# Optimization experiments

Hardware: AMD Instinct MI355X
Metric: run time of the kernel (lower is better)

## Reference

```python
import jax, jax.numpy as jnp
import numpy as np

B, T, S, L_SRC, V, H, E, AV = 16, 128, 192, 192, 30522, 768, 768, 200
L_ORG = L_SRC - 1
KEEP, DEL, STOP, PAD = 3, 4, 2, 0  # SP_IDS = [KEEP, DEL, INSERT, STOP, PAD, LEFT, RIGHT, MARK]


def lstm(x, Wih, Whh, bih, bhh):
    # x: [B, T, E] -> outputs [B, T, H]; PyTorch gate order i, f, g, o
    Bx = x.shape[0]
    Hh = Whh.shape[1]
    def step(carry, xt):
        h, c = carry
        g = xt @ Wih.T + bih + h @ Whh.T + bhh
        i, f, gg, o = jnp.split(g, 4, axis=-1)
        c = jax.nn.sigmoid(f) * c + jax.nn.sigmoid(i) * jnp.tanh(gg)
        h = jax.nn.sigmoid(o) * jnp.tanh(c)
        return (h, c), h
    h0 = jnp.zeros((Bx, Hh), x.dtype)
    _, hs = jax.lax.scan(step, (h0, h0), jnp.swapaxes(x, 0, 1))
    return jnp.swapaxes(hs, 0, 1)


def compute_counters(input_edits, org_ids):
    # Vectorized replica of the host-side numpy counter bookkeeping.
    # Emits the PRE-update counters used at each timestep t (updated with gold = input_edits[:, t+1]).
    Bx = input_edits.shape[0]
    golds = jnp.swapaxes(input_edits[:, 1:], 0, 1)  # [T-1, B]
    barange = jnp.arange(Bx)
    Lorg = org_ids.shape[1]
    def step(carry, g):
        cd, ci, ca = carry
        pre = (cd, ci, ca)
        cd2 = cd + ((g == KEEP) | (g == DEL)).astype(jnp.int32)
        alive = (g != DEL) & (g != STOP) & (g != PAD)
        ci2 = ci + alive.astype(jnp.int32)
        nxt = jnp.clip(ca + 1, 0, Lorg - 1)
        tok = org_ids[barange, nxt]
        cond = alive & (g != KEEP) & (ca + 1 < Lorg) & ((tok == 103) | (tok == 3) | (tok == 4))
        ca2 = jnp.where(cond, ca + 1, jnp.maximum(cd2, ca))
        return (cd2, ci2, ca2), pre
    z = jnp.zeros((Bx,), jnp.int32)
    _, (cds, cis, cas) = jax.lax.scan(step, (z, z, z), golds)
    return jnp.swapaxes(cds, 0, 1), jnp.swapaxes(cis, 0, 1), jnp.swapaxes(cas, 0, 1)  # each [B, T-1]


def setup_inputs():
    key = jax.random.key(0)
    ks = jax.random.split(key, 40)
    s = 0.02
    rn = lambda k, sh: jax.random.normal(k, sh, jnp.float32) * s
    inp = {
        "input_edits": jax.random.randint(ks[0], (B, T), 0, 12),
        "input_actions": jax.random.randint(ks[1], (B, T), 0, AV),
        "simp_sent": jax.random.randint(ks[2], (B, S), 0, V),
        "org_ids": jax.random.randint(ks[3], (B, L_ORG), 0, V),
        "encoder_outputs_org": jax.random.normal(ks[4], (B, L_SRC, H), jnp.float32),
        "emb": rn(ks[5], (V, E)),
    }
    i = 6
    for nm in ("e", "a", "w"):
        inp["Wih_" + nm] = rn(ks[i], (4 * H, E)); i += 1
        inp["Whh_" + nm] = rn(ks[i], (4 * H, H)); i += 1
        inp["bih_" + nm] = jnp.zeros((4 * H,), jnp.float32)
        inp["bhh_" + nm] = jnp.zeros((4 * H,), jnp.float32)
    inp["W_align"] = rn(ks[i], (H, H)); i += 1
    inp["W_proj"] = rn(ks[i], (H, H)); i += 1
    inp["W_ref"] = rn(ks[i], (2, H)); i += 1
    inp["b_ref"] = jnp.zeros((2,), jnp.float32)
    inp["W_mlp"] = rn(ks[i], (E, 5 * H)); i += 1
    inp["b_mlp"] = jnp.zeros((E,), jnp.float32)
    inp["W_act"] = rn(ks[i], (E, 5 * H)); i += 1
    inp["b_act"] = jnp.zeros((E,), jnp.float32)
    inp["W_out"] = rn(ks[i], (V, E)); i += 1
    inp["b_out"] = jnp.zeros((V,), jnp.float32)
    inp["W_outact"] = rn(ks[i], (AV, E)); i += 1
    inp["b_outact"] = jnp.zeros((AV,), jnp.float32)
    m = np.full((1, AV), -100000.0, dtype=np.float32)
    m[0, [0, 1, 2, 5, 101, 102]] = 0.0
    inp["action_mask"] = jnp.asarray(m)
    return inp


def reference(input_edits, input_actions, simp_sent, org_ids, encoder_outputs_org, emb,
              Wih_e, Whh_e, bih_e, bhh_e, Wih_a, Whh_a, bih_a, bhh_a, Wih_w, Whh_w, bih_w, bhh_w,
              W_align, W_proj, W_ref, b_ref, W_mlp, b_mlp, W_act, b_act,
              W_out, b_out, W_outact, b_outact, action_mask):
    # tanh(output_hidden_alignment(enc)) then drop the first (CLS) position
    enc = jnp.tanh(encoder_outputs_org @ W_align.T)[:, 1:]  # [B, L_ORG, H]
    out_e = lstm(emb[input_edits], Wih_e, Whh_e, bih_e, bhh_e)
    out_a = lstm(emb[input_actions], Wih_a, Whh_a, bih_a, bhh_a)
    out_w = lstm(emb[simp_sent], Wih_w, Whh_w, bih_w, bhh_w)
    cd, ci, ca = compute_counters(input_edits, org_ids)  # [B, T-1] each
    Tm1 = input_edits.shape[1] - 1
    bidx = jnp.arange(enc.shape[0])[:, None]
    c_input = enc[bidx, cd]   # [B, T-1, H] data-dependent gather per timestep
    c_anno = enc[bidx, ca]
    c_word = out_w[bidx, ci]
    dec_e = out_e[:, :Tm1]
    dec_a = out_a[:, :Tm1]
    c_pair = jnp.stack([c_input, c_anno], axis=2)  # [B, T-1, 2, H]
    wref_e = jax.nn.softmax(dec_e @ W_ref.T + b_ref, axis=-1)
    wref_a = jax.nn.softmax(dec_a @ W_ref.T + b_ref, axis=-1)
    c_edit = jnp.einsum('btk,btkh->bth', wref_e, c_pair)
    c_action = jnp.einsum('btk,btkh->bth', wref_a, c_pair)
    attn = jax.nn.softmax(jnp.einsum('bth,blh->btl', c_word @ W_proj.T, enc), axis=-1)
    applied = jnp.einsum('btl,blh->bth', attn, enc)
    feat_a = jnp.concatenate([dec_a, dec_e, applied, c_action, c_word], axis=-1)
    act_log = jax.nn.log_softmax(jnp.tanh(feat_a @ W_act.T + b_act) @ W_outact.T + b_outact + action_mask[0], axis=-1)
    feat_e = jnp.concatenate([dec_e, dec_a, applied, c_edit, c_word], axis=-1)
    edit_log = jax.nn.log_softmax(jnp.tanh(feat_e @ W_mlp.T + b_mlp) @ W_out.T + b_out, axis=-1)
    return edit_log, act_log
```

## Files before the change

### kernel.cpp

```cpp
#include <hip/hip_runtime.h>
#include <hip/hip_bf16.h>

typedef __hip_bfloat16 bf16;

#define B_    16
#define T_    128
#define S_    192
#define H_    768
#define G4_   3072
#define V_    30522
#define AV_   200
#define L_    191
#define TM1_  127
#define R_    2032
#define K5_   3840
#define NB_   48
#define HSL_  16
#define NCV_  96

typedef short bf16x8_t __attribute__((ext_vector_type(8)));
typedef float f32x4_t  __attribute__((ext_vector_type(4)));

__device__ __forceinline__ float bf2f(bf16 v) { return __bfloat162float(v); }
__device__ __forceinline__ bf16  f2bf(float v) { return __float2bfloat16(v); }
__device__ __forceinline__ unsigned short f2us(float v) { bf16 h = f2bf(v); return *reinterpret_cast<unsigned short*>(&h); }
__device__ __forceinline__ float uslo(unsigned u) { union { unsigned i; float f; } x; x.i = u << 16; return x.f; }
__device__ __forceinline__ float ushi(unsigned u) { union { unsigned i; float f; } x; x.i = u & 0xffff0000u; return x.f; }
__device__ __forceinline__ float us2f(unsigned short u) { union { unsigned i; float f; } x; x.i = ((unsigned)u) << 16; return x.f; }
__device__ __forceinline__ float sigm(float x) { return 1.0f / (1.0f + expf(-x)); }

#define GLDS(gptr, lptr) \
    __builtin_amdgcn_global_load_lds((const __attribute__((address_space(1))) void*)(gptr), \
                                     (__attribute__((address_space(3))) void*)(lptr), 16, 0, 0)

__global__ __launch_bounds__(256) void gemm_mfma(
    const bf16* __restrict__ A, const bf16* __restrict__ W,
    const float* __restrict__ bias1, const float* __restrict__ bias2,
    bf16* __restrict__ Ch, float* __restrict__ Cf,
    int M, int N, int K, int act, int rowdiv, int lda)
{
    __shared__ short As[128 * 64];
    __shared__ short Ws[128 * 64];
    const int tid = threadIdx.x;
    const int wave = tid >> 6, lane = tid & 63;
    const int mw = (wave >> 1) * 64, nw = (wave & 1) * 64;
    const int bm = blockIdx.x * 128, bn = blockIdx.y * 128;

    const int schunk = (lane & 7) ^ (lane >> 3);

    const bf16* aSrc[4];
    const bf16* wSrc[4];
#pragma unroll
    for (int j = 0; j < 4; ++j) {
        const int idx = wave * 4 + j;
        const int srow = idx * 8 + (lane >> 3);
        int ga = bm + srow; if (ga > M - 1) ga = M - 1;
        const int ra = (rowdiv > 0) ? (ga + ga / rowdiv + 1) : ga;
        aSrc[j] = A + (size_t)ra * lda + schunk * 8;
        int gw = bn + srow; if (gw > N - 1) gw = N - 1;
        wSrc[j] = W + (size_t)gw * K + schunk * 8;
    }

    f32x4_t acc[4][4];
#pragma unroll
    for (int mi = 0; mi < 4; ++mi)
#pragma unroll
        for (int ni = 0; ni < 4; ++ni) acc[mi][ni] = (f32x4_t){0.f, 0.f, 0.f, 0.f};

    const int fr = lane & 15;
    const int fr7 = fr & 7;
    const int cq = lane >> 4;

    for (int k0 = 0; k0 < K; k0 += 64) {
#pragma unroll
        for (int j = 0; j < 4; ++j) {
            const int idx = wave * 4 + j;
            GLDS(aSrc[j] + k0, &As[idx * 512]);
            GLDS(wSrc[j] + k0, &Ws[idx * 512]);
        }
        __syncthreads();
#pragma unroll
        for (int half = 0; half < 2; ++half) {
            const int gc = half * 4 + cq;
            const int lc = (gc ^ fr7) * 8;
            bf16x8_t af[4], wf[4];
#pragma unroll
            for (int i = 0; i < 4; ++i)
                af[i] = *(const bf16x8_t*)&As[(mw + i * 16 + fr) * 64 + lc];
#pragma unroll
            for (int i = 0; i < 4; ++i)
                wf[i] = *(const bf16x8_t*)&Ws[(nw + i * 16 + fr) * 64 + lc];
#pragma unroll
            for (int mi = 0; mi < 4; ++mi)
#pragma unroll
                for (int ni = 0; ni < 4; ++ni)
                    acc[mi][ni] = __builtin_amdgcn_mfma_f32_16x16x32_bf16(af[mi], wf[ni], acc[mi][ni], 0, 0, 0);
        }
        __syncthreads();
    }

    const int cl = lane & 15;
    const int rg = (lane >> 4) * 4;
#pragma unroll
    for (int mi = 0; mi < 4; ++mi) {
#pragma unroll
        for (int ni = 0; ni < 4; ++ni) {
            const int col = bn + nw + ni * 16 + cl;
            if (col >= N) continue;
#pragma unroll
            for (int j = 0; j < 4; ++j) {
                const int row = bm + mw + mi * 16 + rg + j;
                if (row >= M) continue;
                float v = acc[mi][ni][j];
                if (bias1) v += bias1[col];
                if (bias2) v += bias2[col];
                if (act == 1) v = tanhf(v);
                if (Ch) Ch[(size_t)row * N + col] = f2bf(v);
                else    Cf[(size_t)row * N + col] = v;
            }
        }
    }
}

struct ConvJobs {
    const float* src[9];
    bf16* dst[9];
    int n4[9];
};
__global__ void conv_many_kernel(ConvJobs jobs)
{
    const int w = blockIdx.y;
    const int i = blockIdx.x * 256 + threadIdx.x;
    if (i >= jobs.n4[w]) return;
    const float* s = jobs.src[w];
    bf16* d = jobs.dst[w];
    float4 v = *(const float4*)(s + (size_t)i * 4);
    ushort4 o;
    o.x = f2us(v.x); o.y = f2us(v.y); o.z = f2us(v.z); o.w = f2us(v.w);
    *(ushort4*)(d + (size_t)i * 4) = o;
}

__global__ __launch_bounds__(256) void lstm_mfma_kernel(
    const bf16* __restrict__ pxe, const bf16* __restrict__ pxa, const bf16* __restrict__ pxw,
    const float* __restrict__ We, const float* __restrict__ Wa, const float* __restrict__ Ww,
    bf16* __restrict__ oute, bf16* __restrict__ outa, bf16* __restrict__ outw,
    unsigned short* __restrict__ hbuf, int* __restrict__ flags,
    const float* __restrict__ Wout, bf16* __restrict__ Wob)
{
    const int tid = threadIdx.x;

    if (blockIdx.x >= 3 * NB_) {
        const int wid = blockIdx.x - 3 * NB_;
        const int n4 = V_ * H_ / 4;
        for (int i = wid * 256 + tid; i < n4; i += NCV_ * 256) {
            float4 v = *(const float4*)(Wout + (size_t)i * 4);
            ushort4 o;
            o.x = f2us(v.x); o.y = f2us(v.y); o.z = f2us(v.z); o.w = f2us(v.w);
            *(ushort4*)(Wob + (size_t)i * 4) = o;
        }
        return;
    }

    const int which = blockIdx.x / NB_;
    const int nb = blockIdx.x % NB_;
    const bf16* px; const float* W; bf16* out; int Tn;
    if (which == 0)      { px = pxe; W = We; out = oute; Tn = T_; }
    else if (which == 1) { px = pxa; W = Wa; out = outa; Tn = T_; }
    else                 { px = pxw; W = Ww; out = outw; Tn = S_; }
    unsigned short* hG = hbuf + (size_t)which * (2 * B_ * H_);
    int* flg = flags + which * 64;

    const int wv = tid >> 6;
    const int lane = tid & 63;
    const int so = nb * HSL_;

    __shared__ unsigned short hL[16][776];
    __shared__ float gS[4][16][17];
    __shared__ unsigned short oring[8][16][16];

    bf16x8_t Afrag[24];
    {
        const int m = lane & 15;
        const int kb8 = (lane >> 4) * 8;
        const float* wrow = W + (size_t)(wv * H_ + so + m) * H_ + kb8;
#pragma unroll
        for (int kb = 0; kb < 24; ++kb) {
            float4 f0 = *(const float4*)(wrow + kb * 32);
            float4 f1 = *(const float4*)(wrow + kb * 32 + 4);
            bf16x8_t a;
            a[0] = (short)f2us(f0.x); a[1] = (short)f2us(f0.y);
            a[2] = (short)f2us(f0.z); a[3] = (short)f2us(f0.w);
            a[4] = (short)f2us(f1.x); a[5] = (short)f2us(f1.y);
            a[6] = (short)f2us(f1.z); a[7] = (short)f2us(f1.w);
            Afrag[kb] = a;
        }
    }

    for (int i = tid; i < 16 * 776; i += 256) ((unsigned short*)hL)[i] = 0;

    const int cb = tid >> 4;
    const int chl = tid & 15;
    float c = 0.f;

    const int bn = lane & 15;
    const int bk = (lane >> 4) * 8;

    unsigned short pxr0, pxr1, pxr2, pxr3;
    {
        const bf16* q = px + ((size_t)cb * Tn + 0) * G4_ + so + chl;
        pxr0 = *(const unsigned short*)(q);
        pxr1 = *(const unsigned short*)(q + H_);
        pxr2 = *(const unsigned short*)(q + 2 * H_);
        pxr3 = *(const unsigned short*)(q + 3 * H_);
    }

    int cur = 0;
    for (int step = 0; step < Tn; ++step) {
        if (step > 0) {
            const unsigned long long* hsrc =
                (const unsigned long long*)(hG + (size_t)cur * (B_ * H_));
            for (int i = tid; i < B_ * H_ / 4; i += 256) {
                const unsigned long long v =
                    __hip_atomic_load(hsrc + i, __ATOMIC_RELAXED, __HIP_MEMORY_SCOPE_AGENT);
                const int bb = i / (H_ / 4);
                const int cc = i - bb * (H_ / 4);
                ((unsigned long long*)&hL[bb][0])[cc] = v;
            }
        }
        __syncthreads();

        f32x4_t acc = {0.f, 0.f, 0.f, 0.f};
#pragma unroll
        for (int kb = 0; kb < 24; ++kb) {
            bf16x8_t bfr = *(const bf16x8_t*)&hL[bn][kb * 32 + bk];
            acc = __builtin_amdgcn_mfma_f32_16x16x32_bf16(Afrag[kb], bfr, acc, 0, 0, 0);
        }
        {
            const int m0 = (lane >> 4) * 4;
#pragma unroll
            for (int j = 0; j < 4; ++j) gS[wv][m0 + j][bn] = acc[j];
        }
        __syncthreads();

        {
            const float gi = gS[0][chl][cb] + us2f(pxr0);
            const float gf = gS[1][chl][cb] + us2f(pxr1);
            const float gg = gS[2][chl][cb] + us2f(pxr2);
            const float go = gS[3][chl][cb] + us2f(pxr3);
            const float cn = sigm(gf) * c + sigm(gi) * tanhf(gg);
            const float hn = sigm(go) * tanhf(cn);
            c = cn;
            oring[step & 7][cb][chl] = f2us(hn);
            __hip_atomic_store(&hG[(size_t)(cur ^ 1) * (B_ * H_) + cb * H_ + so + chl],
                               f2us(hn), __ATOMIC_RELAXED, __HIP_MEMORY_SCOPE_AGENT);
        }

        if (step + 1 < Tn) {
            __syncthreads();
            const int target = step + 1;
            if (tid == 0)
                __hip_atomic_store(&flg[nb], target, __ATOMIC_RELAXED, __HIP_MEMORY_SCOPE_AGENT);
            {
                const bf16* q = px + ((size_t)cb * Tn + target) * G4_ + so + chl;
                pxr0 = *(const unsigned short*)(q);
                pxr1 = *(const unsigned short*)(q + H_);
                pxr2 = *(const unsigned short*)(q + 2 * H_);
                pxr3 = *(const unsigned short*)(q + 3 * H_);
            }
            if ((step & 7) == 7) {
                const int base = step & ~7;
                for (int s2 = 0; s2 < 8; ++s2)
                    out[((size_t)cb * Tn + base + s2) * H_ + so + chl] =
                        *reinterpret_cast<const bf16*>(&oring[s2][cb][chl]);
            }
            if (lane < NB_) {
                long guard = 0;
                while (__hip_atomic_load(&flg[lane], __ATOMIC_RELAXED, __HIP_MEMORY_SCOPE_AGENT) < target) {
                    __builtin_amdgcn_s_sleep(1);
                    if (++guard > 50000000L) break;
                }
            }
        } else {
            const int base = step & ~7;
            const int cnt8 = (step & 7) + 1;
            for (int s2 = 0; s2 < cnt8; ++s2)
                out[((size_t)cb * Tn + base + s2) * H_ + so + chl] =
                    *reinterpret_cast<const bf16*>(&oring[s2][cb][chl]);
        }
        cur ^= 1;
    }
}

__global__ void gather3_kernel(const int* __restrict__ ids_e, const int* __restrict__ ids_a,
                               const int* __restrict__ ids_w, const float* __restrict__ emb,
                               bf16* __restrict__ oe, bf16* __restrict__ oa,
                               bf16* __restrict__ ow)
{
    const int which = blockIdx.y;
    const int r = blockIdx.x;
    const int* ids; bf16* out; int nr;
    if (which == 0)      { ids = ids_e; out = oe; nr = B_ * T_; }
    else if (which == 1) { ids = ids_a; out = oa; nr = B_ * T_; }
    else                 { ids = ids_w; out = ow; nr = B_ * S_; }
    if (r >= nr) return;
    const float4* src = (const float4*)(emb + (size_t)ids[r] * H_);
    ushort4* dst = (ushort4*)(out + (size_t)r * H_);
    for (int h = threadIdx.x; h < H_ / 4; h += 256) {
        float4 v = src[h];
        ushort4 o;
        o.x = f2us(v.x); o.y = f2us(v.y); o.z = f2us(v.z); o.w = f2us(v.w);
        dst[h] = o;
    }
}

__global__ void counters_kernel(const int* __restrict__ edits, const int* __restrict__ org,
                                int* __restrict__ cd, int* __restrict__ ci, int* __restrict__ ca)
{
    const int b = threadIdx.x;
    if (b >= B_) return;
    int vd = 0, vi = 0, va = 0;
    for (int t = 0; t < TM1_; ++t) {
        cd[b * TM1_ + t] = vd; ci[b * TM1_ + t] = vi; ca[b * TM1_ + t] = va;
        const int g = edits[b * T_ + t + 1];
        const int vd2 = vd + ((g == 3 || g == 4) ? 1 : 0);
        const int alive = (g != 4 && g != 2 && g != 0) ? 1 : 0;
        const int vi2 = vi + alive;
        int nxt = va + 1; if (nxt > L_ - 1) nxt = L_ - 1;
        const int tok = org[b * L_ + nxt];
        const bool cond = alive && (g != 3) && (va + 1 < L_) && (tok == 103 || tok == 3 || tok == 4);
        const int va2 = cond ? (va + 1) : max(vd2, va);
        vd = vd2; vi = vi2; va = va2;
    }
}

__global__ void gather_cword_kernel(const bf16* __restrict__ outw, const int* __restrict__ ci,
                                    bf16* __restrict__ cw)
{
    const int r = blockIdx.x;
    const int b = r / TM1_;
    const unsigned* src = (const unsigned*)(outw + ((size_t)b * S_ + ci[r]) * H_);
    unsigned* dst = (unsigned*)(cw + (size_t)r * H_);
    for (int h = threadIdx.x; h < H_ / 2; h += 256) dst[h] = src[h];
}

__global__ __launch_bounds__(256) void ref_combine_kernel(
    const bf16* __restrict__ oute, const bf16* __restrict__ outa, const bf16* __restrict__ enc,
    const float* __restrict__ Wref, const float* __restrict__ bref,
    const int* __restrict__ cd, const int* __restrict__ ca,
    bf16* __restrict__ ced, bf16* __restrict__ cac)
{
    const int r = blockIdx.x;
    const int b = r / TM1_;
    const int t = r % TM1_;
    const bf16* de = oute + ((size_t)b * T_ + t) * H_;
    const bf16* da = outa + ((size_t)b * T_ + t) * H_;
    const int tid = threadIdx.x;
    __shared__ float red[256][4];
    float s0 = 0.f, s1 = 0.f, s2 = 0.f, s3 = 0.f;
    for (int k = tid; k < H_; k += 256) {
        const float w0 = Wref[k];
        const float w1 = Wref[H_ + k];
        const float e = bf2f(de[k]);
        const float a = bf2f(da[k]);
        s0 += e * w0; s1 += e * w1; s2 += a * w0; s3 += a * w1;
    }
    red[tid][0] = s0; red[tid][1] = s1; red[tid][2] = s2; red[tid][3] = s3;
    __syncthreads();
    for (int off = 128; off > 0; off >>= 1) {
        if (tid < off) {
            red[tid][0] += red[tid + off][0];
            red[tid][1] += red[tid + off][1];
            red[tid][2] += red[tid + off][2];
            red[tid][3] += red[tid + off][3];
        }
        __syncthreads();
    }
    const float br0 = bref[0], br1 = bref[1];
    const float xe0 = red[0][0] + br0, xe1 = red[0][1] + br1;
    const float xa0 = red[0][2] + br0, xa1 = red[0][3] + br1;
    const float me = fmaxf(xe0, xe1);
    const float ee0 = expf(xe0 - me), ee1 = expf(xe1 - me);
    const float pe0 = ee0 / (ee0 + ee1), pe1 = ee1 / (ee0 + ee1);
    const float ma = fmaxf(xa0, xa1);
    const float ea0 = expf(xa0 - ma), ea1 = expf(xa1 - ma);
    const float pa0 = ea0 / (ea0 + ea1), pa1 = ea1 / (ea0 + ea1);

    const bf16* ei = enc + ((size_t)b * L_ + cd[r]) * H_;
    const bf16* ea = enc + ((size_t)b * L_ + ca[r]) * H_;
    for (int h = tid; h < H_; h += 256) {
        const float vi = bf2f(ei[h]);
        const float va = bf2f(ea[h]);
        ced[(size_t)r * H_ + h] = f2bf(pe0 * vi + pe1 * va);
        cac[(size_t)r * H_ + h] = f2bf(pa0 * vi + pa1 * va);
    }
}

__global__ __launch_bounds__(256) void attn_kernel(const bf16* __restrict__ q,
                                                   const bf16* __restrict__ enc,
                                                   bf16* __restrict__ app)
{
    const int r = blockIdx.x;
    const int b = r / TM1_;
    const int tid = threadIdx.x;
    __shared__ float qs[H_];
    __shared__ float p[L_ + 1];
    __shared__ float red[256];
    const bf16* qrow = q + (size_t)r * H_;
    for (int h = tid; h < H_; h += 256) qs[h] = bf2f(qrow[h]);
    __syncthreads();
    const bf16* eb = enc + (size_t)b * L_ * H_;
    float myv = -1e30f;
    if (tid < L_) {
        const unsigned* er = (const unsigned*)(eb + (size_t)tid * H_);
        float s = 0.f;
        for (int k2 = 0; k2 < H_ / 2; ++k2) {
            const unsigned u = er[k2];
            s += qs[2 * k2] * uslo(u) + qs[2 * k2 + 1] * ushi(u);
        }
        p[tid] = s;
        myv = s;
    }
    red[tid] = myv;
    __syncthreads();
    for (int off = 128; off > 0; off >>= 1) {
        if (tid < off) red[tid] = fmaxf(red[tid], red[tid + off]);
        __syncthreads();
    }
    const float m = red[0];
    __syncthreads();
    float e = 0.f;
    if (tid < L_) e = expf(p[tid] - m);
    red[tid] = e;
    __syncthreads();
    for (int off = 128; off > 0; off >>= 1) {
        if (tid < off) red[tid] += red[tid + off];
        __syncthreads();
    }
    const float invZ = 1.f / red[0];
    __syncthreads();
    if (tid < L_) p[tid] = e * invZ;
    __syncthreads();
    for (int h = tid; h < H_; h += 256) {
        float s = 0.f;
        for (int l = 0; l < L_; ++l) s += p[l] * bf2f(eb[(size_t)l * H_ + h]);
        app[(size_t)r * H_ + h] = f2bf(s);
    }
}

__global__ void feat_kernel(const bf16* __restrict__ oute, const bf16* __restrict__ outa,
                            const bf16* __restrict__ app, const bf16* __restrict__ ced,
                            const bf16* __restrict__ cac, const bf16* __restrict__ cw,
                            bf16* __restrict__ fe, bf16* __restrict__ fa)
{
    const int r = blockIdx.x;
    const int b = r / TM1_;
    const int t = r % TM1_;
    const unsigned* de  = (const unsigned*)(oute + ((size_t)b * T_ + t) * H_);
    const unsigned* da  = (const unsigned*)(outa + ((size_t)b * T_ + t) * H_);
    const unsigned* ap  = (const unsigned*)(app + (size_t)r * H_);
    const unsigned* ce  = (const unsigned*)(ced + (size_t)r * H_);
    const unsigned* cA  = (const unsigned*)(cac + (size_t)r * H_);
    const unsigned* cwp = (const unsigned*)(cw + (size_t)r * H_);
    unsigned* pfe = (unsigned*)(fe + (size_t)r * K5_);
    unsigned* pfa = (unsigned*)(fa + (size_t)r * K5_);
    const int HW = H_ / 2;
    for (int h = threadIdx.x; h < HW; h += 256) {
        const unsigned ve = de[h], va = da[h], vap = ap[h], vce = ce[h], vca = cA[h], vcw = cwp[h];
        pfe[h] = ve;  pfe[HW + h] = va;  pfe[2 * HW + h] = vap; pfe[3 * HW + h] = vce; pfe[4 * HW + h] = vcw;
        pfa[h] = va;  pfa[HW + h] = ve;  pfa[2 * HW + h] = vap; pfa[3 * HW + h] = vca; pfa[4 * HW + h] = vcw;
    }
}

__global__ __launch_bounds__(1024) void logsoftmax_edit_kernel(float* __restrict__ out)
{
    float* row = out + (size_t)blockIdx.x * V_;
    const int tid = threadIdx.x;
    const int lane = tid & 63;
    const int wid = tid >> 6;
    __shared__ unsigned short rowb[V_];
    __shared__ float wredm[16], wreds[16];
    __shared__ float fin;

    float m = -1e30f, s = 0.f;
    for (int i = tid; i < V_; i += 1024) {
        const float x = row[i];
        rowb[i] = f2us(x);
        if (x > m) { s = s * expf(m - x) + 1.f; m = x; }
        else s += expf(x - m);
    }
#pragma unroll
    for (int off = 32; off > 0; off >>= 1) {
        const float m2 = __shfl_down(m, off);
        const float s2 = __shfl_down(s, off);
        const float mn = fmaxf(m, m2);
        s = s * expf(m - mn) + s2 * expf(m2 - mn);
        m = mn;
    }
    if (lane == 0) { wredm[wid] = m; wreds[wid] = s; }
    __syncthreads();
    if (wid == 0) {
        m = (lane < 16) ? wredm[lane] : -1e30f;
        s = (lane < 16) ? wreds[lane] : 0.f;
#pragma unroll
        for (int off = 8; off > 0; off >>= 1) {
            const float m2 = __shfl_down(m, off);
            const float s2 = __shfl_down(s, off);
            const float mn = fmaxf(m, m2);
            s = s * expf(m - mn) + s2 * expf(m2 - mn);
            m = mn;
        }
        if (lane == 0) fin = m + logf(s);
    }
    __syncthreads();
    const float lz = fin;
    for (int i = tid; i < V_; i += 1024) row[i] = us2f(rowb[i]) - lz;
}

__global__ __launch_bounds__(256) void logsoftmax_act_kernel(const float* __restrict__ in,
                                                             float* __restrict__ out)
{
    const float* row = in + (size_t)blockIdx.x * AV_;
    float* orow = out + (size_t)blockIdx.x * AV_;
    const int tid = threadIdx.x;
    __shared__ float red[256];
    float m = -1e30f;
    if (tid < AV_) m = row[tid];
    red[tid] = m;
    __syncthreads();
    for (int off = 128; off > 0; off >>= 1) {
        if (tid < off) red[tid] = fmaxf(red[tid], red[tid + off]);
        __syncthreads();
    }
    m = red[0];
    __syncthreads();
    float s = 0.f;
    if (tid < AV_) s = expf(row[tid] - m);
    red[tid] = s;
    __syncthreads();
    for (int off = 128; off > 0; off >>= 1) {
        if (tid < off) red[tid] += red[tid + off];
        __syncthreads();
    }
    const float lz = m + logf(red[0]);
    if (tid < AV_) orow[tid] = row[tid] - lz;
}

extern "C" void kernel_launch(void* const* d_in, const int* in_sizes, int n_in,
                              void* d_out, int out_size, void* d_ws, size_t ws_size,
                              hipStream_t stream)
{
    const int* input_edits   = (const int*)d_in[0];
    const int* input_actions = (const int*)d_in[1];
    const int* simp_sent     = (const int*)d_in[2];
    const int* org_ids       = (const int*)d_in[3];
    const float* enc_org     = (const float*)d_in[4];
    const float* emb         = (const float*)d_in[5];
    const float* Wih_e = (const float*)d_in[6];
    const float* Whh_e = (const float*)d_in[7];
    const float* bih_e = (const float*)d_in[8];
    const float* bhh_e = (const float*)d_in[9];
    const float* Wih_a = (const float*)d_in[10];
    const float* Whh_a = (const float*)d_in[11];
    const float* bih_a = (const float*)d_in[12];
    const float* bhh_a = (const float*)d_in[13];
    const float* Wih_w = (const float*)d_in[14];
    const float* Whh_w = (const float*)d_in[15];
    const float* bih_w = (const float*)d_in[16];
    const float* bhh_w = (const float*)d_in[17];
    const float* W_align = (const float*)d_in[18];
    const float* W_proj  = (const float*)d_in[19];
    const float* W_ref   = (const float*)d_in[20];
    const float* b_ref   = (const float*)d_in[21];
    const float* W_mlp   = (const float*)d_in[22];
    const float* b_mlp   = (const float*)d_in[23];
    const float* W_act   = (const float*)d_in[24];
    const float* b_act   = (const float*)d_in[25];
    const float* W_out   = (const float*)d_in[26];
    const float* b_out   = (const float*)d_in[27];
    const float* W_outact = (const float*)d_in[28];
    const float* b_outact = (const float*)d_in[29];
    const float* action_mask = (const float*)d_in[30];

    float* out = (float*)d_out;
    float* edit_out = out;
    float* act_out  = out + (size_t)R_ * V_;

    char* p = (char*)d_ws;
    auto take = [&](size_t bytes) { void* q = (void*)p; p += ((bytes + 255) / 256) * 256; return q; };
    int* flags = (int*)take(3 * 256);
    unsigned short* hbuf = (unsigned short*)take((size_t)3 * 2 * B_ * H_ * 2);
    char* alias_base = p;
    bf16* xe   = (bf16*)take((size_t)B_ * T_ * H_ * 2);
    bf16* xa   = (bf16*)take((size_t)B_ * T_ * H_ * 2);
    bf16* xw   = (bf16*)take((size_t)B_ * S_ * H_ * 2);
    bf16* pxe  = (bf16*)take((size_t)B_ * T_ * G4_ * 2);
    bf16* pxa  = (bf16*)take((size_t)B_ * T_ * G4_ * 2);
    bf16* pxw  = (bf16*)take((size_t)B_ * S_ * G4_ * 2);
    bf16* oute = (bf16*)take((size_t)B_ * T_ * H_ * 2);
    bf16* outa = (bf16*)take((size_t)B_ * T_ * H_ * 2);
    bf16* outw = (bf16*)take((size_t)B_ * S_ * H_ * 2);
    bf16* enc  = (bf16*)take((size_t)B_ * L_ * H_ * 2);
    bf16* cw   = (bf16*)take((size_t)R_ * H_ * 2);
    bf16* ced  = (bf16*)take((size_t)R_ * H_ * 2);
    bf16* cac  = (bf16*)take((size_t)R_ * H_ * 2);
    bf16* qb   = (bf16*)take((size_t)R_ * H_ * 2);
    bf16* app  = (bf16*)take((size_t)R_ * H_ * 2);
    bf16* fe   = (bf16*)take((size_t)R_ * K5_ * 2);
    bf16* fa   = (bf16*)take((size_t)R_ * K5_ * 2);
    bf16* he   = (bf16*)take((size_t)R_ * H_ * 2);
    bf16* ha   = (bf16*)take((size_t)R_ * H_ * 2);
    int*  cd   = (int*)take((size_t)R_ * 4);
    int*  ci   = (int*)take((size_t)R_ * 4);
    int*  ca   = (int*)take((size_t)R_ * 4);
    float* actbuf = (float*)take((size_t)R_ * AV_ * 4);
    bf16* Wmlpb = (bf16*)take((size_t)H_ * K5_ * 2);
    bf16* Wactb = (bf16*)take((size_t)H_ * K5_ * 2);
    bf16* Woab  = (bf16*)take((size_t)AV_ * H_ * 2);
    bf16* Wob = (bf16*)alias_base;
    bf16* WihEb = fe;
    bf16* WihAb = fe + (size_t)G4_ * H_;
    bf16* WihWb = fe + (size_t)2 * G4_ * H_;
    bf16* encb   = fa;
    bf16* Walb   = fa + (size_t)B_ * S_ * H_;
    bf16* Wprojb = fa + (size_t)B_ * S_ * H_ + (size_t)H_ * H_;

    hipMemsetAsync(flags, 0, 3 * 256, stream);

    ConvJobs jobs;
    jobs.src[0] = Wih_e;   jobs.dst[0] = WihEb;  jobs.n4[0] = G4_ * H_ / 4;
    jobs.src[1] = Wih_a;   jobs.dst[1] = WihAb;  jobs.n4[1] = G4_ * H_ / 4;
    jobs.src[2] = Wih_w;   jobs.dst[2] = WihWb;  jobs.n4[2] = G4_ * H_ / 4;
    jobs.src[3] = W_mlp;   jobs.dst[3] = Wmlpb;  jobs.n4[3] = H_ * K5_ / 4;
    jobs.src[4] = W_act;   jobs.dst[4] = Wactb;  jobs.n4[4] = H_ * K5_ / 4;
    jobs.src[5] = enc_org; jobs.dst[5] = encb;   jobs.n4[5] = B_ * S_ * H_ / 4;
    jobs.src[6] = W_align; jobs.dst[6] = Walb;   jobs.n4[6] = H_ * H_ / 4;
    jobs.src[7] = W_proj;  jobs.dst[7] = Wprojb; jobs.n4[7] = H_ * H_ / 4;
    jobs.src[8] = W_outact;jobs.dst[8] = Woab;   jobs.n4[8] = AV_ * H_ / 4;
    conv_many_kernel<<<dim3((H_ * K5_ / 4 + 255) / 256, 9), 256, 0, stream>>>(jobs);

    gather3_kernel<<<dim3(B_ * S_, 3), 256, 0, stream>>>(
        input_edits, input_actions, simp_sent, emb, xe, xa, xw);

    dim3 gpx((B_ * T_ + 127) / 128, (G4_ + 127) / 128);
    gemm_mfma<<<gpx, 256, 0, stream>>>(xe, WihEb, bih_e, bhh_e, pxe, nullptr, B_ * T_, G4_, H_, 0, 0, H_);
    gemm_mfma<<<gpx, 256, 0, stream>>>(xa, WihAb, bih_a, bhh_a, pxa, nullptr, B_ * T_, G4_, H_, 0, 0, H_);
    dim3 gpxw((B_ * S_ + 127) / 128, (G4_ + 127) / 128);
    gemm_mfma<<<gpxw, 256, 0, stream>>>(xw, WihWb, bih_w, bhh_w, pxw, nullptr, B_ * S_, G4_, H_, 0, 0, H_);

    dim3 genc((B_ * L_ + 127) / 128, (H_ + 127) / 128);
    gemm_mfma<<<genc, 256, 0, stream>>>(encb, Walb, nullptr, nullptr, enc, nullptr, B_ * L_, H_, H_, 1, L_, H_);

    counters_kernel<<<1, 64, 0, stream>>>(input_edits, org_ids, cd, ci, ca);

    lstm_mfma_kernel<<<3 * NB_ + NCV_, 256, 0, stream>>>(pxe, pxa, pxw, Whh_e, Whh_a, Whh_w,
                                                         oute, outa, outw, hbuf, flags,
                                                         W_out, Wob);

    gather_cword_kernel<<<R_, 256, 0, stream>>>(outw, ci, cw);

    ref_combine_kernel<<<R_, 256, 0, stream>>>(oute, outa, enc, W_ref, b_ref, cd, ca, ced, cac);

    dim3 gproj((R_ + 127) / 128, (H_ + 127) / 128);
    gemm_mfma<<<gproj, 256, 0, stream>>>(cw, Wprojb, nullptr, nullptr, qb, nullptr, R_, H_, H_, 0, 0, H_);

    attn_kernel<<<R_, 256, 0, stream>>>(qb, enc, app);

    feat_kernel<<<R_, 256, 0, stream>>>(oute, outa, app, ced, cac, cw, fe, fa);

    gemm_mfma<<<gproj, 256, 0, stream>>>(fe, Wmlpb, b_mlp, nullptr, he, nullptr, R_, H_, K5_, 1, 0, K5_);
    gemm_mfma<<<gproj, 256, 0, stream>>>(fa, Wactb, b_act, nullptr, ha, nullptr, R_, H_, K5_, 1, 0, K5_);

    dim3 gact((R_ + 127) / 128, (AV_ + 127) / 128);
    gemm_mfma<<<gact, 256, 0, stream>>>(ha, Woab, b_outact, action_mask, nullptr, actbuf, R_, AV_, H_, 0, 0, H_);
    logsoftmax_act_kernel<<<R_, 256, 0, stream>>>(actbuf, act_out);

    dim3 gedit((R_ + 127) / 128, (V_ + 127) / 128);
    gemm_mfma<<<gedit, 256, 0, stream>>>(he, Wob, b_out, nullptr, nullptr, edit_out, R_, V_, H_, 0, 0, H_);
    logsoftmax_edit_kernel<<<R_, 1024, 0, stream>>>(edit_out);
}
```

Before: 2.138 ms.

## Fuse reference-combine, attention and feature assembly; gather c_word rows inside GEMM

Three per-row kernels (ref_combine, attention, feature concat) become one, which writes the concatenated feature rows directly. The c_word gather kernel is removed: the projection GEMM reads outw rows through a per-row index array that the counters kernel now also emits. This drops several launches and the global round-trips through the cw, ced, cac and app intermediate buffers. The GEMM gains an extra pointer check and an indirect row load.

```diff
diff --git a/kernel.cpp b/kernel.cpp
--- a/kernel.cpp
+++ b/kernel.cpp
@@ -37,7 +37,8 @@
     const bf16* __restrict__ A, const bf16* __restrict__ W,
     const float* __restrict__ bias1, const float* __restrict__ bias2,
     bf16* __restrict__ Ch, float* __restrict__ Cf,
-    int M, int N, int K, int act, int rowdiv, int lda)
+    int M, int N, int K, int act, int rowdiv, int lda,
+    const int* __restrict__ gidx)
 {
     __shared__ short As[128 * 64];
     __shared__ short Ws[128 * 64];
@@ -55,7 +56,9 @@
         const int idx = wave * 4 + j;
         const int srow = idx * 8 + (lane >> 3);
         int ga = bm + srow; if (ga > M - 1) ga = M - 1;
-        const int ra = (rowdiv > 0) ? (ga + ga / rowdiv + 1) : ga;
+        int ra;
+        if (gidx) ra = gidx[ga];
+        else ra = (rowdiv > 0) ? (ga + ga / rowdiv + 1) : ga;
         aSrc[j] = A + (size_t)ra * lda + schunk * 8;
         int gw = bn + srow; if (gw > N - 1) gw = N - 1;
         wSrc[j] = W + (size_t)gw * K + schunk * 8;
@@ -314,13 +317,15 @@
 }
 
 __global__ void counters_kernel(const int* __restrict__ edits, const int* __restrict__ org,
-                                int* __restrict__ cd, int* __restrict__ ci, int* __restrict__ ca)
+                                int* __restrict__ cd, int* __restrict__ ci, int* __restrict__ ca,
+                                int* __restrict__ cwrow)
 {
     const int b = threadIdx.x;
     if (b >= B_) return;
     int vd = 0, vi = 0, va = 0;
     for (int t = 0; t < TM1_; ++t) {
         cd[b * TM1_ + t] = vd; ci[b * TM1_ + t] = vi; ca[b * TM1_ + t] = va;
+        cwrow[b * TM1_ + t] = b * S_ + vi;
         const int g = edits[b * T_ + t + 1];
         const int vd2 = vd + ((g == 3 || g == 4) ? 1 : 0);
         const int alive = (g != 4 && g != 2 && g != 0) ? 1 : 0;
@@ -333,51 +338,55 @@
     }
 }
 
-__global__ void gather_cword_kernel(const bf16* __restrict__ outw, const int* __restrict__ ci,
-                                    bf16* __restrict__ cw)
-{
-    const int r = blockIdx.x;
-    const int b = r / TM1_;
-    const unsigned* src = (const unsigned*)(outw + ((size_t)b * S_ + ci[r]) * H_);
-    unsigned* dst = (unsigned*)(cw + (size_t)r * H_);
-    for (int h = threadIdx.x; h < H_ / 2; h += 256) dst[h] = src[h];
-}
-
-__global__ __launch_bounds__(256) void ref_combine_kernel(
-    const bf16* __restrict__ oute, const bf16* __restrict__ outa, const bf16* __restrict__ enc,
+__global__ __launch_bounds__(256) void fused_row_kernel(
+    const bf16* __restrict__ oute, const bf16* __restrict__ outa,
+    const bf16* __restrict__ enc, const bf16* __restrict__ outw,
+    const bf16* __restrict__ qb,
     const float* __restrict__ Wref, const float* __restrict__ bref,
     const int* __restrict__ cd, const int* __restrict__ ca,
-    bf16* __restrict__ ced, bf16* __restrict__ cac)
+    const int* __restrict__ cwrow,
+    bf16* __restrict__ fe, bf16* __restrict__ fa)
 {
     const int r = blockIdx.x;
     const int b = r / TM1_;
     const int t = r % TM1_;
+    const int tid = threadIdx.x;
     const bf16* de = oute + ((size_t)b * T_ + t) * H_;
     const bf16* da = outa + ((size_t)b * T_ + t) * H_;
-    const int tid = threadIdx.x;
-    __shared__ float red[256][4];
-    float s0 = 0.f, s1 = 0.f, s2 = 0.f, s3 = 0.f;
-    for (int k = tid; k < H_; k += 256) {
-        const float w0 = Wref[k];
-        const float w1 = Wref[H_ + k];
-        const float e = bf2f(de[k]);
-        const float a = bf2f(da[k]);
-        s0 += e * w0; s1 += e * w1; s2 += a * w0; s3 += a * w1;
-    }
-    red[tid][0] = s0; red[tid][1] = s1; red[tid][2] = s2; red[tid][3] = s3;
+
+    __shared__ float red4[256][4];
+    __shared__ float qs[H_];
+    __shared__ float p[L_ + 1];
+    __shared__ float red[256];
+
+    {
+        float s0 = 0.f, s1 = 0.f, s2 = 0.f, s3 = 0.f;
+        for (int k = tid; k < H_; k += 256) {
+            const float w0 = Wref[k];
+            const float w1 = Wref[H_ + k];
+            const float e = bf2f(de[k]);
+            const float a = bf2f(da[k]);
+            s0 += e * w0; s1 += e * w1; s2 += a * w0; s3 += a * w1;
+        }
+        red4[tid][0] = s0; red4[tid][1] = s1; red4[tid][2] = s2; red4[tid][3] = s3;
+    }
+    {
+        const bf16* qrow = qb + (size_t)r * H_;
+        for (int h = tid; h < H_; h += 256) qs[h] = bf2f(qrow[h]);
+    }
     __syncthreads();
     for (int off = 128; off > 0; off >>= 1) {
         if (tid < off) {
-            red[tid][0] += red[tid + off][0];
-            red[tid][1] += red[tid + off][1];
-            red[tid][2] += red[tid + off][2];
-            red[tid][3] += red[tid + off][3];
+            red4[tid][0] += red4[tid + off][0];
+            red4[tid][1] += red4[tid + off][1];
+            red4[tid][2] += red4[tid + off][2];
+            red4[tid][3] += red4[tid + off][3];
         }
         __syncthreads();
     }
     const float br0 = bref[0], br1 = bref[1];
-    const float xe0 = red[0][0] + br0, xe1 = red[0][1] + br1;
-    const float xa0 = red[0][2] + br0, xa1 = red[0][3] + br1;
+    const float xe0 = red4[0][0] + br0, xe1 = red4[0][1] + br1;
+    const float xa0 = red4[0][2] + br0, xa1 = red4[0][3] + br1;
     const float me = fmaxf(xe0, xe1);
     const float ee0 = expf(xe0 - me), ee1 = expf(xe1 - me);
     const float pe0 = ee0 / (ee0 + ee1), pe1 = ee1 / (ee0 + ee1);
@@ -385,29 +394,6 @@
     const float ea0 = expf(xa0 - ma), ea1 = expf(xa1 - ma);
     const float pa0 = ea0 / (ea0 + ea1), pa1 = ea1 / (ea0 + ea1);
 
-    const bf16* ei = enc + ((size_t)b * L_ + cd[r]) * H_;
-    const bf16* ea = enc + ((size_t)b * L_ + ca[r]) * H_;
-    for (int h = tid; h < H_; h += 256) {
-        const float vi = bf2f(ei[h]);
-        const float va = bf2f(ea[h]);
-        ced[(size_t)r * H_ + h] = f2bf(pe0 * vi + pe1 * va);
-        cac[(size_t)r * H_ + h] = f2bf(pa0 * vi + pa1 * va);
-    }
-}
-
-__global__ __launch_bounds__(256) void attn_kernel(const bf16* __restrict__ q,
-                                                   const bf16* __restrict__ enc,
-                                                   bf16* __restrict__ app)
-{
-    const int r = blockIdx.x;
-    const int b = r / TM1_;
-    const int tid = threadIdx.x;
-    __shared__ float qs[H_];
-    __shared__ float p[L_ + 1];
-    __shared__ float red[256];
-    const bf16* qrow = q + (size_t)r * H_;
-    for (int h = tid; h < H_; h += 256) qs[h] = bf2f(qrow[h]);
-    __syncthreads();
     const bf16* eb = enc + (size_t)b * L_ * H_;
     float myv = -1e30f;
     if (tid < L_) {
@@ -440,34 +426,25 @@
     __syncthreads();
     if (tid < L_) p[tid] = e * invZ;
     __syncthreads();
+
+    const bf16* ecd = enc + ((size_t)b * L_ + cd[r]) * H_;
+    const bf16* eca = enc + ((size_t)b * L_ + ca[r]) * H_;
+    const bf16* cwp = outw + (size_t)cwrow[r] * H_;
+    bf16* pfe = fe + (size_t)r * K5_;
+    bf16* pfa = fa + (size_t)r * K5_;
     for (int h = tid; h < H_; h += 256) {
-        float s = 0.f;
-        for (int l = 0; l < L_; ++l) s += p[l] * bf2f(eb[(size_t)l * H_ + h]);
-        app[(size_t)r * H_ + h] = f2bf(s);
-    }
-}
-
-__global__ void feat_kernel(const bf16* __restrict__ oute, const bf16* __restrict__ outa,
-                            const bf16* __restrict__ app, const bf16* __restrict__ ced,
-                            const bf16* __restrict__ cac, const bf16* __restrict__ cw,
-                            bf16* __restrict__ fe, bf16* __restrict__ fa)
-{
-    const int r = blockIdx.x;
-    const int b = r / TM1_;
-    const int t = r % TM1_;
-    const unsigned* de  = (const unsigned*)(oute + ((size_t)b * T_ + t) * H_);
-    const unsigned* da  = (const unsigned*)(outa + ((size_t)b * T_ + t) * H_);
-    const unsigned* ap  = (const unsigned*)(app + (size_t)r * H_);
-    const unsigned* ce  = (const unsigned*)(ced + (size_t)r * H_);
-    const unsigned* cA  = (const unsigned*)(cac + (size_t)r * H_);
-    const unsigned* cwp = (const unsigned*)(cw + (size_t)r * H_);
-    unsigned* pfe = (unsigned*)(fe + (size_t)r * K5_);
-    unsigned* pfa = (unsigned*)(fa + (size_t)r * K5_);
-    const int HW = H_ / 2;
-    for (int h = threadIdx.x; h < HW; h += 256) {
-        const unsigned ve = de[h], va = da[h], vap = ap[h], vce = ce[h], vca = cA[h], vcw = cwp[h];
-        pfe[h] = ve;  pfe[HW + h] = va;  pfe[2 * HW + h] = vap; pfe[3 * HW + h] = vce; pfe[4 * HW + h] = vcw;
-        pfa[h] = va;  pfa[HW + h] = ve;  pfa[2 * HW + h] = vap; pfa[3 * HW + h] = vca; pfa[4 * HW + h] = vcw;
+        float appv = 0.f;
+        for (int l = 0; l < L_; ++l) appv += p[l] * bf2f(eb[(size_t)l * H_ + h]);
+        const bf16 appb = f2bf(appv);
+        const float vi = bf2f(ecd[h]);
+        const float va = bf2f(eca[h]);
+        const bf16 cedv = f2bf(pe0 * vi + pe1 * va);
+        const bf16 cacv = f2bf(pa0 * vi + pa1 * va);
+        const bf16 dev = de[h], dav = da[h], cwv = cwp[h];
+        pfe[h] = dev;  pfe[H_ + h] = dav;  pfe[2 * H_ + h] = appb;
+        pfe[3 * H_ + h] = cedv;  pfe[4 * H_ + h] = cwv;
+        pfa[h] = dav;  pfa[H_ + h] = dev;  pfa[2 * H_ + h] = appb;
+        pfa[3 * H_ + h] = cacv;  pfa[4 * H_ + h] = cwv;
     }
 }
 
@@ -600,11 +577,7 @@
     bf16* outa = (bf16*)take((size_t)B_ * T_ * H_ * 2);
     bf16* outw = (bf16*)take((size_t)B_ * S_ * H_ * 2);
     bf16* enc  = (bf16*)take((size_t)B_ * L_ * H_ * 2);
-    bf16* cw   = (bf16*)take((size_t)R_ * H_ * 2);
-    bf16* ced  = (bf16*)take((size_t)R_ * H_ * 2);
-    bf16* cac  = (bf16*)take((size_t)R_ * H_ * 2);
     bf16* qb   = (bf16*)take((size_t)R_ * H_ * 2);
-    bf16* app  = (bf16*)take((size_t)R_ * H_ * 2);
     bf16* fe   = (bf16*)take((size_t)R_ * K5_ * 2);
     bf16* fa   = (bf16*)take((size_t)R_ * K5_ * 2);
     bf16* he   = (bf16*)take((size_t)R_ * H_ * 2);
@@ -612,6 +585,7 @@
     int*  cd   = (int*)take((size_t)R_ * 4);
     int*  ci   = (int*)take((size_t)R_ * 4);
     int*  ca   = (int*)take((size_t)R_ * 4);
+    int*  cwrow = (int*)take((size_t)R_ * 4);
     float* actbuf = (float*)take((size_t)R_ * AV_ * 4);
     bf16* Wmlpb = (bf16*)take((size_t)H_ * K5_ * 2);
     bf16* Wactb = (bf16*)take((size_t)H_ * K5_ * 2);
@@ -642,39 +616,34 @@
         input_edits, input_actions, simp_sent, emb, xe, xa, xw);
 
     dim3 gpx((B_ * T_ + 127) / 128, (G4_ + 127) / 128);
-    gemm_mfma<<<gpx, 256, 0, stream>>>(xe, WihEb, bih_e, bhh_e, pxe, nullptr, B_ * T_, G4_, H_, 0, 0, H_);
-    gemm_mfma<<<gpx, 256, 0, stream>>>(xa, WihAb, bih_a, bhh_a, pxa, nullptr, B_ * T_, G4_, H_, 0, 0, H_);
+    gemm_mfma<<<gpx, 256, 0, stream>>>(xe, WihEb, bih_e, bhh_e, pxe, nullptr, B_ * T_, G4_, H_, 0, 0, H_, nullptr);
+    gemm_mfma<<<gpx, 256, 0, stream>>>(xa, WihAb, bih_a, bhh_a, pxa, nullptr, B_ * T_, G4_, H_, 0, 0, H_, nullptr);
     dim3 gpxw((B_ * S_ + 127) / 128, (G4_ + 127) / 128);
-    gemm_mfma<<<gpxw, 256, 0, stream>>>(xw, WihWb, bih_w, bhh_w, pxw, nullptr, B_ * S_, G4_, H_, 0, 0, H_);
+    gemm_mfma<<<gpxw, 256, 0, stream>>>(xw, WihWb, bih_w, bhh_w, pxw, nullptr, B_ * S_, G4_, H_, 0, 0, H_, nullptr);
 
     dim3 genc((B_ * L_ + 127) / 128, (H_ + 127) / 128);
-    gemm_mfma<<<genc, 256, 0, stream>>>(encb, Walb, nullptr, nullptr, enc, nullptr, B_ * L_, H_, H_, 1, L_, H_);
-
-    counters_kernel<<<1, 64, 0, stream>>>(input_edits, org_ids, cd, ci, ca);
+    gemm_mfma<<<genc, 256, 0, stream>>>(encb, Walb, nullptr, nullptr, enc, nullptr, B_ * L_, H_, H_, 1, L_, H_, nullptr);
+
+    counters_kernel<<<1, 64, 0, stream>>>(input_edits, org_ids, cd, ci, ca, cwrow);
 
     lstm_mfma_kernel<<<3 * NB_ + NCV_, 256, 0, stream>>>(pxe, pxa, pxw, Whh_e, Whh_a, Whh_w,
                                                          oute, outa, outw, hbuf, flags,
                                                          W_out, Wob);
 
-    gather_cword_kernel<<<R_, 256, 0, stream>>>(outw, ci, cw);
-
-    ref_combine_kernel<<<R_, 256, 0, stream>>>(oute, outa, enc, W_ref, b_ref, cd, ca, ced, cac);
-
     dim3 gproj((R_ + 127) / 128, (H_ + 127) / 128);
-    gemm_mfma<<<gproj, 256, 0, stream>>>(cw, Wprojb, nullptr, nullptr, qb, nullptr, R_, H_, H_, 0, 0, H_);
-
-    attn_kernel<<<R_, 256, 0, stream>>>(qb, enc, app);
-
-    feat_kernel<<<R_, 256, 0, stream>>>(oute, outa, app, ced, cac, cw, fe, fa);
-
-    gemm_mfma<<<gproj, 256, 0, stream>>>(fe, Wmlpb, b_mlp, nullptr, he, nullptr, R_, H_, K5_, 1, 0, K5_);
-    gemm_mfma<<<gproj, 256, 0, stream>>>(fa, Wactb, b_act, nullptr, ha, nullptr, R_, H_, K5_, 1, 0, K5_);
+    gemm_mfma<<<gproj, 256, 0, stream>>>(outw, Wprojb, nullptr, nullptr, qb, nullptr, R_, H_, H_, 0, 0, H_, cwrow);
+
+    fused_row_kernel<<<R_, 256, 0, stream>>>(oute, outa, enc, outw, qb,
+                                             W_ref, b_ref, cd, ca, cwrow, fe, fa);
+
+    gemm_mfma<<<gproj, 256, 0, stream>>>(fe, Wmlpb, b_mlp, nullptr, he, nullptr, R_, H_, K5_, 1, 0, K5_, nullptr);
+    gemm_mfma<<<gproj, 256, 0, stream>>>(fa, Wactb, b_act, nullptr, ha, nullptr, R_, H_, K5_, 1, 0, K5_, nullptr);
 
     dim3 gact((R_ + 127) / 128, (AV_ + 127) / 128);
-    gemm_mfma<<<gact, 256, 0, stream>>>(ha, Woab, b_outact, action_mask, nullptr, actbuf, R_, AV_, H_, 0, 0, H_);
+    gemm_mfma<<<gact, 256, 0, stream>>>(ha, Woab, b_outact, action_mask, nullptr, actbuf, R_, AV_, H_, 0, 0, H_, nullptr);
     logsoftmax_act_kernel<<<R_, 256, 0, stream>>>(actbuf, act_out);
 
     dim3 gedit((R_ + 127) / 128, (V_ + 127) / 128);
-    gemm_mfma<<<gedit, 256, 0, stream>>>(he, Wob, b_out, nullptr, nullptr, edit_out, R_, V_, H_, 0, 0, H_);
+    gemm_mfma<<<gedit, 256, 0, stream>>>(he, Wob, b_out, nullptr, nullptr, edit_out, R_, V_, H_, 0, 0, H_, nullptr);
     logsoftmax_edit_kernel<<<R_, 1024, 0, stream>>>(edit_out);
 }
```

Result: no change. 2.162 ms (+1.2%).
